# Kernel tuning notes

Hardware: AMD Instinct MI355X
Metric: run time of the kernel (lower is better)

Reference implementation:

```python
import jax, jax.numpy as jnp
import numpy as np

N = 50000
E = 800000
H = 8
DH = 32  # hidden 256 / heads 8


def gat_layer(h, src, dst, W, a_src, a_dst, b):
    # h: [N, 256] -> per-head projected features [N, H, DH]
    hp = (h @ W).reshape(N, H, DH)
    # per-node attention logits for src/dst roles: [N, H]
    s_src = jnp.einsum('nhd,hd->nh', hp, a_src)
    s_dst = jnp.einsum('nhd,hd->nh', hp, a_dst)
    e = jax.nn.leaky_relu(s_src[src] + s_dst[dst], negative_slope=0.2)  # [Et, H]
    # segment softmax over incoming edges of each dst node
    m = jax.ops.segment_max(e, dst, num_segments=N)  # [N, H]
    ex = jnp.exp(e - m[dst])
    denom = jax.ops.segment_sum(ex, dst, num_segments=N)  # [N, H] (>0: self-loops)
    alpha = ex / denom[dst]  # [Et, H]
    out = jax.ops.segment_sum(alpha[:, :, None] * hp[src], dst, num_segments=N)
    return out.reshape(N, H * DH) + b


def han_forward(x, edges, proj_W, proj_b, gat_W, gat_asrc, gat_adst, gat_b,
                sem_W1, sem_b1, sem_W2, cls_W1, cls_b1, cls_W2, cls_b2):
    h0 = x @ proj_W + proj_b  # [N, 256]
    loop = jnp.arange(N, dtype=edges.dtype)
    embs = []
    for p in range(edges.shape[0]):  # 3 meta-paths (fixed, small)
        src = jnp.concatenate([edges[p, 0], loop])  # add self-loops (PyG default)
        dst = jnp.concatenate([edges[p, 1], loop])
        h = h0
        for l in range(2):  # 2 GAT layers per meta-path
            h = gat_layer(h, src, dst, gat_W[p, l], gat_asrc[p, l], gat_adst[p, l], gat_b[p, l])
            h = jax.nn.elu(h)  # dropout: eval-mode no-op
        embs.append(h)
    emb = jnp.stack(embs, axis=1)  # [N, P, 256]
    scores = (jnp.tanh(emb @ sem_W1 + sem_b1) @ sem_W2).squeeze(-1)  # [N, P]
    w = jax.nn.softmax(scores, axis=1)
    z = jnp.sum(emb * w[:, :, None], axis=1)  # [N, 256]
    hcls = jax.nn.relu(z @ cls_W1 + cls_b1)
    logits = hcls @ cls_W2 + cls_b2  # [N, 2]
    return logits


def setup_inputs() -> dict:
    key = jax.random.key(0)
    ks = jax.random.split(key, 16)
    s = 0.05
    return {
        'x': jax.random.normal(ks[0], (N, 128), jnp.float32),
        'edges': jax.random.randint(ks[1], (3, 2, E), 0, N, dtype=jnp.int32),
        'proj_W': jax.random.normal(ks[2], (128, 256), jnp.float32) * s,
        'proj_b': jnp.zeros((256,), jnp.float32),
        'gat_W': jax.random.normal(ks[3], (3, 2, 256, 256), jnp.float32) * s,
        'gat_asrc': jax.random.normal(ks[4], (3, 2, H, DH), jnp.float32) * s,
        'gat_adst': jax.random.normal(ks[5], (3, 2, H, DH), jnp.float32) * s,
        'gat_b': jnp.zeros((3, 2, 256), jnp.float32),
        'sem_W1': jax.random.normal(ks[6], (256, 128), jnp.float32) * s,
        'sem_b1': jnp.zeros((128,), jnp.float32),
        'sem_W2': jax.random.normal(ks[7], (128, 1), jnp.float32) * s,
        'cls_W1': jax.random.normal(ks[8], (256, 128), jnp.float32) * s,
        'cls_b1': jnp.zeros((128,), jnp.float32),
        'cls_W2': jax.random.normal(ks[9], (128, 2), jnp.float32) * s,
        'cls_b2': jnp.zeros((2,), jnp.float32),
    }


def reference(x, edges, proj_W, proj_b, gat_W, gat_asrc, gat_adst, gat_b,
              sem_W1, sem_b1, sem_W2, cls_W1, cls_b1, cls_W2, cls_b2):
    return han_forward(x, edges, proj_W, proj_b, gat_W, gat_asrc, gat_adst, gat_b,
                       sem_W1, sem_b1, sem_W2, cls_W1, cls_b1, cls_W2, cls_b2)
```

## Files before the change

### kernel.cpp

```cpp
#include <hip/hip_runtime.h>
#include <hip/hip_fp16.h>
#include <math.h>

#define N_NODES 50000
#define N_EDG   800000
#define NH      8
#define DH      32
#define HID     256
#define MAXD    64
#define EPB     4096
#define PROJ_FB 88
#define PROJ_EB (176*EPB)
#define G3_FB   69
#define AGGB    12500

typedef __attribute__((ext_vector_type(8))) short bf16x8;
typedef __attribute__((ext_vector_type(4))) float f32x4;

#define GLL16(src, dst) __builtin_amdgcn_global_load_lds(                  \
    (const __attribute__((address_space(1))) void*)(const void*)(src),     \
    (__attribute__((address_space(3))) void*)(dst), 16, 0, 0)

__device__ __forceinline__ unsigned short f2bf(float x) {
    unsigned u = __float_as_uint(x);
    u += 0x7FFF + ((u >> 16) & 1);
    return (unsigned short)(u >> 16);
}
__device__ __forceinline__ float bf2f(unsigned short h) {
    return __uint_as_float(((unsigned)h) << 16);
}
__device__ __forceinline__ unsigned cvtpk_bf16(float a, float b) {
    unsigned r;
    asm("v_cvt_pk_bf16_f32 %0, %1, %2" : "=v"(r) : "v"(a), "v"(b));
    return r;
}
__device__ __forceinline__ float fastrcp(float x) {
    float r;
    asm("v_rcp_f32 %0, %1" : "=v"(r) : "v"(x));
    return r;
}
__device__ __forceinline__ void split8(const float4& a, const float4& b,
                                       uint4& hi, uint4& lo) {
    float f[8] = {a.x,a.y,a.z,a.w,b.x,b.y,b.z,b.w};
    unsigned hpk[4], lpk[4];
    #pragma unroll
    for (int i = 0; i < 4; ++i) {
        hpk[i] = cvtpk_bf16(f[2*i], f[2*i+1]);
        float hl = __uint_as_float(hpk[i] << 16);
        float hh = __uint_as_float(hpk[i] & 0xffff0000u);
        lpk[i] = cvtpk_bf16(f[2*i] - hl, f[2*i+1] - hh);
    }
    hi = make_uint4(hpk[0], hpk[1], hpk[2], hpk[3]);
    lo = make_uint4(lpk[0], lpk[1], lpk[2], lpk[3]);
}
__device__ __forceinline__ void h8_to_pair(uint4 r, uint4& hi, uint4& lo) {
    const __half2* hp = (const __half2*)&r;
    unsigned hpk[4], lpk[4];
    #pragma unroll
    for (int i = 0; i < 4; ++i) {
        float2 f = __half22float2(hp[i]);
        hpk[i] = cvtpk_bf16(f.x, f.y);
        float hl = __uint_as_float(hpk[i] << 16);
        float hh = __uint_as_float(hpk[i] & 0xffff0000u);
        lpk[i] = cvtpk_bf16(f.x - hl, f.y - hh);
    }
    hi = make_uint4(hpk[0], hpk[1], hpk[2], hpk[3]);
    lo = make_uint4(lpk[0], lpk[1], lpk[2], lpk[3]);
}

__device__ __forceinline__ void fmix2(float& alo, float& ahi, unsigned rv, float w) {
    asm("v_fma_mix_f32 %0, %1, %2, %0 op_sel:[0,0,0] op_sel_hi:[1,0,0]"
        : "+v"(alo) : "v"(rv), "v"(w));
    asm("v_fma_mix_f32 %0, %1, %2, %0 op_sel:[1,0,0] op_sel_hi:[1,0,0]"
        : "+v"(ahi) : "v"(rv), "v"(w));
}

__device__ __forceinline__ void fill_edges(const int* __restrict__ edges,
                                           int* __restrict__ cnt3,
                                           unsigned short* __restrict__ slots3,
                                           int fb, int ebase) {
    const int base = ebase + fb * EPB + (int)threadIdx.x;
    #pragma unroll 1
    for (int t = 0; t < 4; ++t) {
        int dd[4], ss[4];
        #pragma unroll
        for (int j = 0; j < 4; ++j) {
            int e = base + (t * 4 + j) * 256;
            if (e < 3 * N_EDG) {
                int p = e / N_EDG, i = e - p * N_EDG;
                const int* src = edges + (size_t)p * 2 * N_EDG;
                int s = src[i], d = src[N_EDG + i];
                ss[j] = min(max(s, 0), N_NODES - 1);
                dd[j] = p * N_NODES + min(max(d, 0), N_NODES - 1);
            } else { ss[j] = -1; dd[j] = 0; }
        }
        int pos[4];
        #pragma unroll
        for (int j = 0; j < 4; ++j)
            if (ss[j] >= 0) pos[j] = atomicAdd(&cnt3[dd[j]], 1);
        #pragma unroll
        for (int j = 0; j < 4; ++j)
            if (ss[j] >= 0 && pos[j] < MAXD)
                slots3[(size_t)dd[j] * MAXD + pos[j]] = (unsigned short)ss[j];
    }
}

__device__ __forceinline__ void agg_worker(
    int fb, int p, int l,
    const int* __restrict__ cnt3, const unsigned short* __restrict__ slots3,
    const float* __restrict__ ssrc3, const float* __restrict__ sdst3,
    const __half* __restrict__ hp3, const float* __restrict__ gatB,
    __half* __restrict__ emb16) {
    const int wid  = fb * 4 + ((int)threadIdx.x >> 6);
    const int lane = threadIdx.x & 63;
    if (wid >= N_NODES) return;
    const int n = wid;
    const unsigned short* srcs = slots3 + ((size_t)p * N_NODES + n) * MAXD;
    const float* s_src = ssrc3 + p * N_NODES * NH;
    const float* s_dst = sdst3 + p * N_NODES * NH;
    const __half* hp = hp3 + (size_t)p * N_NODES * HID;
    const float* bias = gatB + (2*p + l) * HID;
    const int deg = min(cnt3[p * N_NODES + n], MAXD);

    const int sub = lane & 31, eo = lane >> 5;
    const int h2  = sub >> 2;
    const float sd2 = s_dst[n*NH + h2];
    const uint4* hp4 = (const uint4*)hp;
    float dn = 0.f;
    float a0=0.f,a1=0.f,a2=0.f,a3=0.f,a4=0.f,a5=0.f,a6=0.f,a7=0.f;

    int i = eo;
    for (; i + 6 < deg; i += 8) {
        const int s0 = srcs[i];
        const int s1 = srcs[i + 2];
        const int s2 = srcs[i + 4];
        const int s3 = srcs[i + 6];
        const float x0 = s_src[s0*NH + h2];
        const float x1 = s_src[s1*NH + h2];
        const float x2 = s_src[s2*NH + h2];
        const float x3 = s_src[s3*NH + h2];
        const uint4 r0 = hp4[s0*32 + sub];
        const uint4 r1 = hp4[s1*32 + sub];
        const uint4 r2 = hp4[s2*32 + sub];
        const uint4 r3 = hp4[s3*32 + sub];
        float e0 = x0 + sd2; e0 = e0 > 0.f ? e0 : 0.2f * e0;
        float e1 = x1 + sd2; e1 = e1 > 0.f ? e1 : 0.2f * e1;
        float e2 = x2 + sd2; e2 = e2 > 0.f ? e2 : 0.2f * e2;
        float e3 = x3 + sd2; e3 = e3 > 0.f ? e3 : 0.2f * e3;
        const float w0 = __expf(e0), w1 = __expf(e1);
        const float w2 = __expf(e2), w3 = __expf(e3);
        dn += w0; dn += w1; dn += w2; dn += w3;
        fmix2(a0, a1, r0.x, w0); fmix2(a2, a3, r0.y, w0);
        fmix2(a4, a5, r0.z, w0); fmix2(a6, a7, r0.w, w0);
        fmix2(a0, a1, r1.x, w1); fmix2(a2, a3, r1.y, w1);
        fmix2(a4, a5, r1.z, w1); fmix2(a6, a7, r1.w, w1);
        fmix2(a0, a1, r2.x, w2); fmix2(a2, a3, r2.y, w2);
        fmix2(a4, a5, r2.z, w2); fmix2(a6, a7, r2.w, w2);
        fmix2(a0, a1, r3.x, w3); fmix2(a2, a3, r3.y, w3);
        fmix2(a4, a5, r3.z, w3); fmix2(a6, a7, r3.w, w3);
    }
    for (; i + 2 < deg; i += 4) {
        const int s0 = srcs[i];
        const int s1 = srcs[i + 2];
        const float x0 = s_src[s0*NH + h2];
        const float x1 = s_src[s1*NH + h2];
        const uint4 r0 = hp4[s0*32 + sub];
        const uint4 r1 = hp4[s1*32 + sub];
        float e0 = x0 + sd2; e0 = e0 > 0.f ? e0 : 0.2f * e0;
        float e1 = x1 + sd2; e1 = e1 > 0.f ? e1 : 0.2f * e1;
        const float w0 = __expf(e0), w1 = __expf(e1);
        dn += w0; dn += w1;
        fmix2(a0, a1, r0.x, w0); fmix2(a2, a3, r0.y, w0);
        fmix2(a4, a5, r0.z, w0); fmix2(a6, a7, r0.w, w0);
        fmix2(a0, a1, r1.x, w1); fmix2(a2, a3, r1.y, w1);
        fmix2(a4, a5, r1.z, w1); fmix2(a6, a7, r1.w, w1);
    }
    if (i < deg) {
        const int s0 = srcs[i];
        const float x0 = s_src[s0*NH + h2];
        const uint4 r0 = hp4[s0*32 + sub];
        float e0 = x0 + sd2; e0 = e0 > 0.f ? e0 : 0.2f * e0;
        const float w0 = __expf(e0);
        dn += w0;
        fmix2(a0, a1, r0.x, w0); fmix2(a2, a3, r0.y, w0);
        fmix2(a4, a5, r0.z, w0); fmix2(a6, a7, r0.w, w0);
    }
    dn += __shfl_xor(dn, 32);
    a0 += __shfl_xor(a0, 32); a1 += __shfl_xor(a1, 32);
    a2 += __shfl_xor(a2, 32); a3 += __shfl_xor(a3, 32);
    a4 += __shfl_xor(a4, 32); a5 += __shfl_xor(a5, 32);
    a6 += __shfl_xor(a6, 32); a7 += __shfl_xor(a7, 32);
    if (lane < 32) {
        float evs = s_src[n*NH + h2] + sd2;
        evs = evs > 0.f ? evs : 0.2f * evs;
        float ws = __expf(evs);
        dn += ws;
        const uint4 rs = hp4[n*32 + sub];
        fmix2(a0, a1, rs.x, ws); fmix2(a2, a3, rs.y, ws);
        fmix2(a4, a5, rs.z, ws); fmix2(a6, a7, rs.w, ws);

        float rdn = fastrcp(dn);
        float v[8] = {a0,a1,a2,a3,a4,a5,a6,a7};
        const float4 b0 = *(const float4*)&bias[sub*8];
        const float4 b1 = *(const float4*)&bias[sub*8 + 4];
        v[0]=v[0]*rdn+b0.x; v[1]=v[1]*rdn+b0.y; v[2]=v[2]*rdn+b0.z; v[3]=v[3]*rdn+b0.w;
        v[4]=v[4]*rdn+b1.x; v[5]=v[5]*rdn+b1.y; v[6]=v[6]*rdn+b1.z; v[7]=v[7]*rdn+b1.w;
        unsigned short hh[8];
        #pragma unroll
        for (int k = 0; k < 8; ++k) {
            float e = v[k] > 0.f ? v[k] : (__expf(v[k]) - 1.f);
            hh[k] = __half_as_ushort(__float2half(e));
        }
        size_t o = ((size_t)p * N_NODES + n) * HID + sub * 8;
        *(uint4*)&emb16[o] = make_uint4(hh[0]|((unsigned)hh[1]<<16), hh[2]|((unsigned)hh[3]<<16),
                                        hh[4]|((unsigned)hh[5]<<16), hh[6]|((unsigned)hh[7]<<16));
    }
}

__global__ __launch_bounds__(256)
void agg3y_k(const int* __restrict__ cnt3, const unsigned short* __restrict__ slots3,
             const float* __restrict__ ssrc3, const float* __restrict__ sdst3,
             const __half* __restrict__ hp3, const float* __restrict__ gatB,
             int l, __half* __restrict__ emb16) {
    agg_worker(blockIdx.x, blockIdx.y, l, cnt3, slots3, ssrc3, sdst3, hp3, gatB, emb16);
}

template<int NC, int ACT, int OUTMODE, int AMODE, int FILL>
__global__ __launch_bounds__(256)
void mfma_gemm_k(const float* __restrict__ A32p, const __half* __restrict__ A16p,
                 int lda,
                 const unsigned short* __restrict__ WThi,
                 const unsigned short* __restrict__ WTlo,
                 const float* __restrict__ bias,
                 float* __restrict__ C, __half* __restrict__ Ch,
                 int ldc, int M, int K,
                 const int* __restrict__ edges, int* __restrict__ cnt3,
                 unsigned short* __restrict__ slots3,
                 const float* __restrict__ w4z,
                 int aplanez, int cplanez,
                 const float* __restrict__ logW2, const float* __restrict__ logB2) {
    __shared__ unsigned short sAh[128*32], sAl[128*32], sBh[128*32], sBl[128*32];
    const int gxk = (M + 127) >> 7;
    if constexpr (FILL) {
        if ((int)blockIdx.x >= gxk) {
            fill_edges(edges, cnt3, slots3,
                       ((int)blockIdx.x - gxk) + PROJ_FB * (int)blockIdx.y, 0);
            return;
        }
    }
    if (A16p) A16p += (size_t)blockIdx.z * aplanez;
    if (C)    C    += (size_t)blockIdx.z * cplanez;
    const int tid  = threadIdx.x;
    const int lane = tid & 63;
    const int w    = tid >> 6;
    const int wr   = w >> 1, wc = w & 1;
    const int r0   = blockIdx.x * 128;
    const int c0   = blockIdx.y * 128;
    const int l15  = lane & 15, q = lane >> 4;

    const int cl8   = (((lane & 3) ^ ((lane >> 4) & 3)) << 3);
    const int lrow  = w*32 + (lane >> 2);
    const int gbrow0 = c0 + lrow, gbrow1 = c0 + lrow + 16;
    const int lbase = w * 1024;

    const int srow = tid >> 2, slot = tid & 3;
    const int arow0 = min(r0 + srow,      M - 1);
    const int arow1 = min(r0 + srow + 64, M - 1);
    const size_t ga0 = (size_t)arow0 * lda + slot * 8;
    const size_t ga1 = (size_t)arow1 * lda + slot * 8;
    const int lda0 = srow*32 + ((slot ^ ((srow >> 2) & 3)) << 3);
    const int lda1 = lda0 + 64*32;

    float4 w0r, w1r;
    if constexpr (AMODE == 3) {
        w0r = *(const float4*)&w4z[arow0 * 4];
        w1r = *(const float4*)&w4z[arow1 * 4];
    }

    f32x4 acc[4][4];
    #pragma unroll
    for (int i = 0; i < 4; ++i)
        #pragma unroll
        for (int j = 0; j < 4; ++j) acc[i][j] = (f32x4){0.f, 0.f, 0.f, 0.f};

    const int swzF = (l15 >> 2) & 3;
    const int qs   = ((q ^ swzF) << 3);

    const int nsteps = K >> 5;
    for (int s = 0; s < nsteps; ++s) {
        const int kc = s << 5;
        __syncthreads();
        GLL16(&WThi[(size_t)gbrow0*K + kc + cl8], &sBh[lbase]);
        GLL16(&WThi[(size_t)gbrow1*K + kc + cl8], &sBh[lbase + 512]);
        GLL16(&WTlo[(size_t)gbrow0*K + kc + cl8], &sBl[lbase]);
        GLL16(&WTlo[(size_t)gbrow1*K + kc + cl8], &sBl[lbase + 512]);
        uint4 h0, l0, h1, l1;
        if constexpr (AMODE == 0) {
            float4 f0a = *(const float4*)&A32p[ga0 + kc];
            float4 f0b = *(const float4*)&A32p[ga0 + kc + 4];
            float4 f1a = *(const float4*)&A32p[ga1 + kc];
            float4 f1b = *(const float4*)&A32p[ga1 + kc + 4];
            split8(f0a, f0b, h0, l0);
            split8(f1a, f1b, h1, l1);
        } else if constexpr (AMODE == 1) {
            uint4 r0v = *(const uint4*)&A16p[ga0 + kc];
            uint4 r1v = *(const uint4*)&A16p[ga1 + kc];
            h8_to_pair(r0v, h0, l0);
            h8_to_pair(r1v, h1, l1);
        } else {
            const int off = kc + slot * 8;
            #pragma unroll
            for (int rr = 0; rr < 2; ++rr) {
                const int row = rr ? arow1 : arow0;
                const float4 wv = rr ? w1r : w0r;
                const __half2* e0 = (const __half2*)&A16p[(size_t)row * HID + off];
                const __half2* e1 = (const __half2*)&A16p[((size_t)N_NODES + row) * HID + off];
                const __half2* e2 = (const __half2*)&A16p[((size_t)2*N_NODES + row) * HID + off];
                float vv[8];
                #pragma unroll
                for (int j2 = 0; j2 < 4; ++j2) {
                    float2 fa = __half22float2(e0[j2]);
                    float2 fb2 = __half22float2(e1[j2]);
                    float2 fc = __half22float2(e2[j2]);
                    vv[2*j2]   = wv.x*fa.x + wv.y*fb2.x + wv.z*fc.x;
                    vv[2*j2+1] = wv.x*fa.y + wv.y*fb2.y + wv.z*fc.y;
                }
                if (rr) split8(*(const float4*)&vv[0], *(const float4*)&vv[4], h1, l1);
                else    split8(*(const float4*)&vv[0], *(const float4*)&vv[4], h0, l0);
            }
        }
        *(uint4*)&sAh[lda0] = h0; *(uint4*)&sAl[lda0] = l0;
        *(uint4*)&sAh[lda1] = h1; *(uint4*)&sAl[lda1] = l1;
        __syncthreads();

        bf16x8 fAh[4], fAl[4];
        #pragma unroll
        for (int t = 0; t < 4; ++t) {
            int ra = (wr*64 + t*16 + l15) * 32 + qs;
            fAh[t] = *(const bf16x8*)&sAh[ra];
            fAl[t] = *(const bf16x8*)&sAl[ra];
        }
        #pragma unroll
        for (int nt = 0; nt < 4; ++nt) {
            int rb = (wc*64 + nt*16 + l15) * 32 + qs;
            bf16x8 fBh = *(const bf16x8*)&sBh[rb];
            bf16x8 fBl = *(const bf16x8*)&sBl[rb];
            #pragma unroll
            for (int mt = 0; mt < 4; ++mt) {
                acc[mt][nt] = __builtin_amdgcn_mfma_f32_16x16x32_bf16(fAh[mt], fBh, acc[mt][nt], 0, 0, 0);
                acc[mt][nt] = __builtin_amdgcn_mfma_f32_16x16x32_bf16(fAh[mt], fBl, acc[mt][nt], 0, 0, 0);
                acc[mt][nt] = __builtin_amdgcn_mfma_f32_16x16x32_bf16(fAl[mt], fBh, acc[mt][nt], 0, 0, 0);
            }
        }
    }
    if constexpr (OUTMODE == 3) {
        __syncthreads();
        float* red = (float*)sAh;
        float pl[16][2];
        #pragma unroll
        for (int mt = 0; mt < 4; ++mt)
            #pragma unroll
            for (int r = 0; r < 4; ++r) {
                float p0 = 0.f, p1 = 0.f;
                #pragma unroll
                for (int nt = 0; nt < 4; ++nt) {
                    int col = wc*64 + nt*16 + l15;
                    float v = fmaxf(acc[mt][nt][r] + bias[col], 0.f);
                    p0 += v * logW2[col*2];
                    p1 += v * logW2[col*2 + 1];
                }
                #pragma unroll
                for (int o = 1; o < 16; o <<= 1) {
                    p0 += __shfl_xor(p0, o);
                    p1 += __shfl_xor(p1, o);
                }
                pl[mt*4 + r][0] = p0;
                pl[mt*4 + r][1] = p1;
            }
        if (wc == 1 && l15 == 0) {
            #pragma unroll
            for (int mt = 0; mt < 4; ++mt)
                #pragma unroll
                for (int r = 0; r < 4; ++r) {
                    int rl = wr*64 + mt*16 + q*4 + r;
                    red[rl*2]     = pl[mt*4 + r][0];
                    red[rl*2 + 1] = pl[mt*4 + r][1];
                }
        }
        __syncthreads();
        if (wc == 0 && l15 == 0) {
            #pragma unroll
            for (int mt = 0; mt < 4; ++mt)
                #pragma unroll
                for (int r = 0; r < 4; ++r) {
                    int rl = wr*64 + mt*16 + q*4 + r;
                    int grow = r0 + rl;
                    if (grow < M) {
                        C[(size_t)grow*2]     = pl[mt*4+r][0] + red[rl*2]     + logB2[0];
                        C[(size_t)grow*2 + 1] = pl[mt*4+r][1] + red[rl*2 + 1] + logB2[1];
                    }
                }
        }
        return;
    }
    #pragma unroll
    for (int mt = 0; mt < 4; ++mt)
        #pragma unroll
        for (int nt = 0; nt < 4; ++nt) {
            int col = c0 + wc*64 + nt*16 + l15;
            float bb = bias ? bias[col] : 0.f;
            #pragma unroll
            for (int r = 0; r < 4; ++r) {
                int grow = r0 + wr*64 + mt*16 + q*4 + r;
                if (grow < M) {
                    float v = acc[mt][nt][r] + bb;
                    if (ACT == 1) {
                        float t = __expf(2.f * v);
                        v = 1.f - 2.f * fastrcp(1.f + t);
                    } else if (ACT == 2) v = fmaxf(v, 0.f);
                    size_t o = (size_t)grow * ldc + col;
                    if (OUTMODE == 2) Ch[o] = __float2half(v);
                    else              C[o] = v;
                }
            }
        }
}

template<int FILL>
__global__ __launch_bounds__(256)
void mfma_gemm3_k(const __half* __restrict__ A16p, int aoffz, int lda,
                  const unsigned short* __restrict__ WT, int l,
                  __half* __restrict__ hp3, int M,
                  const int* __restrict__ edges, int* __restrict__ cnt3,
                  unsigned short* __restrict__ slots3) {
    __shared__ unsigned short sAh[128*32], sAl[128*32], sBh[128*32], sBl[128*32];
    const int gx = (M + 127) >> 7;
    if constexpr (FILL) {
        if ((int)blockIdx.x >= gx) {
            fill_edges(edges, cnt3, slots3,
                       ((int)blockIdx.x - gx) + G3_FB * ((int)blockIdx.y + 2 * (int)blockIdx.z),
                       PROJ_EB);
            return;
        }
    }
    const int p = blockIdx.z;
    const __half* Ap = A16p + (size_t)p * aoffz;
    const unsigned short* WThi = WT + (size_t)(2*p + l) * 131072;
    const unsigned short* WTlo = WThi + 65536;
    __half* Ch = hp3 + (size_t)p * N_NODES * HID;
    const int K = HID;

    const int tid  = threadIdx.x;
    const int lane = tid & 63;
    const int w    = tid >> 6;
    const int wr   = w >> 1, wc = w & 1;
    const int r0   = blockIdx.x * 128;
    const int c0   = blockIdx.y * 128;
    const int l15  = lane & 15, q = lane >> 4;

    const int cl8   = (((lane & 3) ^ ((lane >> 4) & 3)) << 3);
    const int lrow  = w*32 + (lane >> 2);
    const int gbrow0 = c0 + lrow, gbrow1 = c0 + lrow + 16;
    const int lbase = w * 1024;

    const int srow = tid >> 2, slot = tid & 3;
    const size_t ga0 = (size_t)min(r0 + srow,      M - 1) * lda + slot * 8;
    const size_t ga1 = (size_t)min(r0 + srow + 64, M - 1) * lda + slot * 8;
    const int lda0 = srow*32 + ((slot ^ ((srow >> 2) & 3)) << 3);
    const int lda1 = lda0 + 64*32;

    f32x4 acc[4][4];
    #pragma unroll
    for (int i = 0; i < 4; ++i)
        #pragma unroll
        for (int j = 0; j < 4; ++j) acc[i][j] = (f32x4){0.f, 0.f, 0.f, 0.f};

    const int swzF = (l15 >> 2) & 3;
    const int qs   = ((q ^ swzF) << 3);

    for (int s = 0; s < 8; ++s) {
        const int kc = s << 5;
        __syncthreads();
        GLL16(&WThi[(size_t)gbrow0*K + kc + cl8], &sBh[lbase]);
        GLL16(&WThi[(size_t)gbrow1*K + kc + cl8], &sBh[lbase + 512]);
        GLL16(&WTlo[(size_t)gbrow0*K + kc + cl8], &sBl[lbase]);
        GLL16(&WTlo[(size_t)gbrow1*K + kc + cl8], &sBl[lbase + 512]);
        uint4 r0v = *(const uint4*)&Ap[ga0 + kc];
        uint4 r1v = *(const uint4*)&Ap[ga1 + kc];
        uint4 h0, l0, h1, l1;
        h8_to_pair(r0v, h0, l0);
        h8_to_pair(r1v, h1, l1);
        *(uint4*)&sAh[lda0] = h0; *(uint4*)&sAl[lda0] = l0;
        *(uint4*)&sAh[lda1] = h1; *(uint4*)&sAl[lda1] = l1;
        __syncthreads();

        bf16x8 fAh[4], fAl[4];
        #pragma unroll
        for (int t = 0; t < 4; ++t) {
            int ra = (wr*64 + t*16 + l15) * 32 + qs;
            fAh[t] = *(const bf16x8*)&sAh[ra];
            fAl[t] = *(const bf16x8*)&sAl[ra];
        }
        #pragma unroll
        for (int nt = 0; nt < 4; ++nt) {
            int rb = (wc*64 + nt*16 + l15) * 32 + qs;
            bf16x8 fBh = *(const bf16x8*)&sBh[rb];
            bf16x8 fBl = *(const bf16x8*)&sBl[rb];
            #pragma unroll
            for (int mt = 0; mt < 4; ++mt) {
                acc[mt][nt] = __builtin_amdgcn_mfma_f32_16x16x32_bf16(fAh[mt], fBh, acc[mt][nt], 0, 0, 0);
                acc[mt][nt] = __builtin_amdgcn_mfma_f32_16x16x32_bf16(fAh[mt], fBl, acc[mt][nt], 0, 0, 0);
                acc[mt][nt] = __builtin_amdgcn_mfma_f32_16x16x32_bf16(fAl[mt], fBh, acc[mt][nt], 0, 0, 0);
            }
        }
    }
    #pragma unroll
    for (int mt = 0; mt < 4; ++mt)
        #pragma unroll
        for (int nt = 0; nt < 4; ++nt) {
            int col = c0 + wc*64 + nt*16 + l15;
            #pragma unroll
            for (int r = 0; r < 4; ++r) {
                int grow = r0 + wr*64 + mt*16 + q*4 + r;
                if (grow < M)
                    Ch[(size_t)grow * HID + col] = __float2half(acc[mt][nt][r]);
            }
        }
}

__global__ __launch_bounds__(256)
void cvtWall_k(const float* __restrict__ gatW, const float* __restrict__ projW,
               const float* __restrict__ semW1, const float* __restrict__ clsW1,
               unsigned short* __restrict__ WT) {
    int y = blockIdx.y;
    const float* W; int K, N;
    if (y < 6)       { W = gatW + (size_t)y * 65536; K = 256; N = 256; }
    else if (y == 6) { W = projW; K = 128; N = 256; }
    else if (y == 7) { W = semW1; K = 256; N = 128; }
    else             { W = clsW1; K = 256; N = 128; }
    int idx = blockIdx.x * 256 + threadIdx.x;
    if (idx >= K * N) return;
    unsigned short* hi = WT + (size_t)y * 131072;
    unsigned short* lo = hi + 65536;
    int k = idx / N, n = idx - k * N;
    float v = W[idx];
    unsigned short h = f2bf(v);
    hi[n * K + k] = h;
    lo[n * K + k] = f2bf(v - bf2f(h));
}

__global__ __launch_bounds__(256)
void attn_scores3_k(const __half* __restrict__ hp3,
                    const float* __restrict__ gatAs, const float* __restrict__ gatAd,
                    int l, int pbase, float* __restrict__ ssrc3, float* __restrict__ sdst3) {
    int p = pbase + blockIdx.y;
    int gid = blockIdx.x * 256 + threadIdx.x;
    if (gid >= N_NODES * NH) return;
    int h = gid & 7;
    const __half2* hv = (const __half2*)(hp3 + (size_t)p * N_NODES * HID + (size_t)gid * DH);
    const float* a = gatAs + (2*p + l) * HID + h * DH;
    const float* d = gatAd + (2*p + l) * HID + h * DH;
    float ss = 0.f, sd = 0.f;
    #pragma unroll
    for (int j = 0; j < 8; ++j) {
        float4 av = ((const float4*)a)[j], dv = ((const float4*)d)[j];
        float2 f0 = __half22float2(hv[2*j]);
        float2 f1 = __half22float2(hv[2*j + 1]);
        ss += f0.x*av.x + f0.y*av.y + f1.x*av.z + f1.y*av.w;
        sd += f0.x*dv.x + f0.y*dv.y + f1.x*dv.z + f1.y*dv.w;
    }
    ssrc3[p * N_NODES * NH + gid] = ss;
    sdst3[p * N_NODES * NH + gid] = sd;
}

__global__ __launch_bounds__(256)
void zero_k(int* p, int n) { int i = blockIdx.x*256 + threadIdx.x; if (i < n) p[i] = 0; }

__global__ __launch_bounds__(256)
void score_w_k(const float* __restrict__ tb, const float* __restrict__ W2,
               float* __restrict__ w4) {
    int wid  = (blockIdx.x * blockDim.x + threadIdx.x) >> 6;
    int lane = threadIdx.x & 63;
    if (wid >= N_NODES) return;
    const int n = wid;
    float sc[3];
    #pragma unroll
    for (int p = 0; p < 3; ++p) {
        const float* tr = tb + (size_t)p * N_NODES * 128 + (size_t)n * 128;
        float part = tr[lane] * W2[lane] + tr[64 + lane] * W2[64 + lane];
        #pragma unroll
        for (int o = 1; o < 64; o <<= 1) part += __shfl_xor(part, o);
        sc[p] = part;
    }
    float m  = fmaxf(sc[0], fmaxf(sc[1], sc[2]));
    float e0 = __expf(sc[0]-m), e1 = __expf(sc[1]-m), e2 = __expf(sc[2]-m);
    float rs = fastrcp(e0 + e1 + e2);
    if (lane == 0)
        *(float4*)&w4[(size_t)n * 4] = make_float4(e0*rs, e1*rs, e2*rs, 0.f);
}

extern "C" void kernel_launch(void* const* d_in, const int* in_sizes, int n_in,
                              void* d_out, int out_size, void* d_ws, size_t ws_size,
                              hipStream_t stream) {
    (void)in_sizes; (void)n_in; (void)out_size; (void)ws_size;
    const float* x     = (const float*)d_in[0];
    const int*   edges = (const int*)  d_in[1];
    const float* projW = (const float*)d_in[2];
    const float* projb = (const float*)d_in[3];
    const float* gatW  = (const float*)d_in[4];
    const float* gatAs = (const float*)d_in[5];
    const float* gatAd = (const float*)d_in[6];
    const float* gatB  = (const float*)d_in[7];
    const float* semW1 = (const float*)d_in[8];
    const float* semb1 = (const float*)d_in[9];
    const float* semW2 = (const float*)d_in[10];
    const float* clsW1 = (const float*)d_in[11];
    const float* clsb1 = (const float*)d_in[12];
    const float* clsW2 = (const float*)d_in[13];
    const float* clsb2 = (const float*)d_in[14];
    float* out = (float*)d_out;

    char* base = (char*)d_ws;
    const size_t PLANE = (size_t)N_NODES * HID * 2;
    __half* hp3   = (__half*)(base);
    __half* emb16 = (__half*)(base + 3*PLANE);
    __half* h016  = (__half*)(base + 6*PLANE);
    char* small = base + 7*PLANE;
    float* ssrc3 = (float*)small;
    float* sdst3 = ssrc3 + 3*(size_t)N_NODES*NH;
    int*   cnt3  = (int*)(sdst3 + 3*(size_t)N_NODES*NH);
    unsigned short* WT = (unsigned short*)(cnt3 + 3*N_NODES);
    unsigned short* slots3 = WT + 9*131072;
    float* w4 = (float*)(slots3 + (size_t)3*N_NODES*MAXD);
    float* t0 = (float*)(base);

    dim3 blk(256);
    const int gx = (N_NODES + 127) / 128;

    cvtWall_k<<<dim3(256, 9), blk, 0, stream>>>(gatW, projW, semW1, clsW1, WT);
    zero_k  <<<(3*N_NODES+255)/256, blk, 0, stream>>>(cnt3, 3*N_NODES);

    mfma_gemm_k<256,0,2,0,1><<<dim3(gx + PROJ_FB, 2), blk, 0, stream>>>(
        x, nullptr, 128, WT + 6*131072, WT + 6*131072 + 65536, projb,
        nullptr, h016, 256, N_NODES, 128, edges, cnt3, slots3, nullptr, 0, 0,
        nullptr, nullptr);

    mfma_gemm3_k<1><<<dim3(gx + G3_FB, 2, 3), blk, 0, stream>>>(
        h016, 0, HID, WT, 0, hp3, N_NODES, edges, cnt3, slots3);

    attn_scores3_k<<<dim3((N_NODES*NH+255)/256, 3), blk, 0, stream>>>(
        hp3, gatAs, gatAd, 0, 0, ssrc3, sdst3);

    agg3y_k<<<dim3(AGGB, 3), blk, 0, stream>>>(
        cnt3, slots3, ssrc3, sdst3, hp3, gatB, 0, emb16);

    mfma_gemm3_k<0><<<dim3(gx, 2, 3), blk, 0, stream>>>(
        emb16, (int)((size_t)N_NODES*HID), HID, WT, 1, hp3, N_NODES,
        nullptr, nullptr, nullptr);

    attn_scores3_k<<<dim3((N_NODES*NH+255)/256, 3), blk, 0, stream>>>(
        hp3, gatAs, gatAd, 1, 0, ssrc3, sdst3);

    agg3y_k<<<dim3(AGGB, 3), blk, 0, stream>>>(
        cnt3, slots3, ssrc3, sdst3, hp3, gatB, 1, emb16);

    mfma_gemm_k<128,1,0,1,0><<<dim3(gx, 1, 3), blk, 0, stream>>>(
        nullptr, emb16, 256, WT + 7*131072, WT + 7*131072 + 65536, semb1,
        t0, nullptr, 128, N_NODES, 256, nullptr, nullptr, nullptr, nullptr,
        (int)((size_t)N_NODES*HID), N_NODES*128, nullptr, nullptr);

    score_w_k<<<dim3(AGGB), blk, 0, stream>>>(t0, semW2, w4);

    mfma_gemm_k<128,2,3,3,0><<<dim3(gx, 1), blk, 0, stream>>>(
        nullptr, emb16, HID, WT + 8*131072, WT + 8*131072 + 65536, clsb1,
        out, nullptr, 0, N_NODES, 256, nullptr, nullptr, nullptr, w4, 0, 0,
        clsW2, clsb2);
}
```

Measured before the change: 942.3 us.

## Fuse attention-score dots into GAT GEMM epilogue and semantic score into sem GEMM

Per-head attention logits (s_src, s_dst) are now computed from the fp32 accumulators in the GAT projection GEMM epilogue with shuffle reductions, which removes the separate attn_scores kernel that re-read the fp16 hp3 planes. The semantic-attention GEMM gains an epilogue that applies tanh, dots with sem_W2 and reduces across the two column waves through LDS. It writes one score per node and metapath straight into w4, replacing the [N,128] intermediate and the wave-per-node score kernel with a small softmax kernel. Scores are now taken from unrounded fp32 accumulators rather than fp16 values, which changes numerics slightly, and the extra epilogue work adds register pressure to the GEMMs.

```diff
diff --git a/kernel.cpp b/kernel.cpp
--- a/kernel.cpp
+++ b/kernel.cpp
@@ -403,6 +403,48 @@
         }
         return;
     }
+    if constexpr (OUTMODE == 4) {
+        __syncthreads();
+        float* red = (float*)sAh;
+        float pl[16];
+        #pragma unroll
+        for (int mt = 0; mt < 4; ++mt)
+            #pragma unroll
+            for (int r = 0; r < 4; ++r) {
+                float pp = 0.f;
+                #pragma unroll
+                for (int nt = 0; nt < 4; ++nt) {
+                    int col = wc*64 + nt*16 + l15;
+                    float v = acc[mt][nt][r] + bias[col];
+                    float t = __expf(2.f * v);
+                    v = 1.f - 2.f * fastrcp(1.f + t);
+                    pp += v * logW2[col];
+                }
+                #pragma unroll
+                for (int o = 1; o < 16; o <<= 1) pp += __shfl_xor(pp, o);
+                pl[mt*4 + r] = pp;
+            }
+        if (wc == 1 && l15 == 0) {
+            #pragma unroll
+            for (int mt = 0; mt < 4; ++mt)
+                #pragma unroll
+                for (int r = 0; r < 4; ++r)
+                    red[wr*64 + mt*16 + q*4 + r] = pl[mt*4 + r];
+        }
+        __syncthreads();
+        if (wc == 0 && l15 == 0) {
+            #pragma unroll
+            for (int mt = 0; mt < 4; ++mt)
+                #pragma unroll
+                for (int r = 0; r < 4; ++r) {
+                    int rl = wr*64 + mt*16 + q*4 + r;
+                    int grow = r0 + rl;
+                    if (grow < M)
+                        C[(size_t)grow*4] = pl[mt*4+r] + red[rl];
+                }
+        }
+        return;
+    }
     #pragma unroll
     for (int mt = 0; mt < 4; ++mt)
         #pragma unroll
@@ -432,7 +474,9 @@
                   const unsigned short* __restrict__ WT, int l,
                   __half* __restrict__ hp3, int M,
                   const int* __restrict__ edges, int* __restrict__ cnt3,
-                  unsigned short* __restrict__ slots3) {
+                  unsigned short* __restrict__ slots3,
+                  const float* __restrict__ gatAs, const float* __restrict__ gatAd,
+                  float* __restrict__ ssrc3, float* __restrict__ sdst3) {
     __shared__ unsigned short sAh[128*32], sAl[128*32], sBh[128*32], sBl[128*32];
     const int gx = (M + 127) >> 7;
     if constexpr (FILL) {
@@ -526,6 +570,42 @@
                     Ch[(size_t)grow * HID + col] = __float2half(acc[mt][nt][r]);
             }
         }
+    {
+        const float* av = gatAs + (2*p + l) * HID;
+        const float* dvv = gatAd + (2*p + l) * HID;
+        float as_[4], ad_[4];
+        #pragma unroll
+        for (int nt = 0; nt < 4; ++nt) {
+            int col = c0 + wc*64 + nt*16 + l15;
+            as_[nt] = av[col];
+            ad_[nt] = dvv[col];
+        }
+        const int hb = (c0 + wc*64) >> 5;
+        #pragma unroll
+        for (int mt = 0; mt < 4; ++mt)
+            #pragma unroll
+            for (int r = 0; r < 4; ++r) {
+                float s0 = acc[mt][0][r]*as_[0] + acc[mt][1][r]*as_[1];
+                float s1 = acc[mt][2][r]*as_[2] + acc[mt][3][r]*as_[3];
+                float d0 = acc[mt][0][r]*ad_[0] + acc[mt][1][r]*ad_[1];
+                float d1 = acc[mt][2][r]*ad_[2] + acc[mt][3][r]*ad_[3];
+                #pragma unroll
+                for (int o = 1; o < 16; o <<= 1) {
+                    s0 += __shfl_xor(s0, o); s1 += __shfl_xor(s1, o);
+                    d0 += __shfl_xor(d0, o); d1 += __shfl_xor(d1, o);
+                }
+                if (l15 == 0) {
+                    int grow = r0 + wr*64 + mt*16 + q*4 + r;
+                    if (grow < M) {
+                        size_t ob = (size_t)p * N_NODES * NH + (size_t)grow * NH;
+                        ssrc3[ob + hb]     = s0;
+                        ssrc3[ob + hb + 1] = s1;
+                        sdst3[ob + hb]     = d0;
+                        sdst3[ob + hb + 1] = d1;
+                    }
+                }
+            }
+    }
 }
 
 __global__ __launch_bounds__(256)
@@ -550,53 +630,17 @@
 }
 
 __global__ __launch_bounds__(256)
-void attn_scores3_k(const __half* __restrict__ hp3,
-                    const float* __restrict__ gatAs, const float* __restrict__ gatAd,
-                    int l, int pbase, float* __restrict__ ssrc3, float* __restrict__ sdst3) {
-    int p = pbase + blockIdx.y;
-    int gid = blockIdx.x * 256 + threadIdx.x;
-    if (gid >= N_NODES * NH) return;
-    int h = gid & 7;
-    const __half2* hv = (const __half2*)(hp3 + (size_t)p * N_NODES * HID + (size_t)gid * DH);
-    const float* a = gatAs + (2*p + l) * HID + h * DH;
-    const float* d = gatAd + (2*p + l) * HID + h * DH;
-    float ss = 0.f, sd = 0.f;
-    #pragma unroll
-    for (int j = 0; j < 8; ++j) {
-        float4 av = ((const float4*)a)[j], dv = ((const float4*)d)[j];
-        float2 f0 = __half22float2(hv[2*j]);
-        float2 f1 = __half22float2(hv[2*j + 1]);
-        ss += f0.x*av.x + f0.y*av.y + f1.x*av.z + f1.y*av.w;
-        sd += f0.x*dv.x + f0.y*dv.y + f1.x*dv.z + f1.y*dv.w;
-    }
-    ssrc3[p * N_NODES * NH + gid] = ss;
-    sdst3[p * N_NODES * NH + gid] = sd;
-}
+void zero_k(int* p, int n) { int i = blockIdx.x*256 + threadIdx.x; if (i < n) p[i] = 0; }
 
 __global__ __launch_bounds__(256)
-void zero_k(int* p, int n) { int i = blockIdx.x*256 + threadIdx.x; if (i < n) p[i] = 0; }
-
-__global__ __launch_bounds__(256)
-void score_w_k(const float* __restrict__ tb, const float* __restrict__ W2,
-               float* __restrict__ w4) {
-    int wid  = (blockIdx.x * blockDim.x + threadIdx.x) >> 6;
-    int lane = threadIdx.x & 63;
-    if (wid >= N_NODES) return;
-    const int n = wid;
-    float sc[3];
-    #pragma unroll
-    for (int p = 0; p < 3; ++p) {
-        const float* tr = tb + (size_t)p * N_NODES * 128 + (size_t)n * 128;
-        float part = tr[lane] * W2[lane] + tr[64 + lane] * W2[64 + lane];
-        #pragma unroll
-        for (int o = 1; o < 64; o <<= 1) part += __shfl_xor(part, o);
-        sc[p] = part;
-    }
-    float m  = fmaxf(sc[0], fmaxf(sc[1], sc[2]));
-    float e0 = __expf(sc[0]-m), e1 = __expf(sc[1]-m), e2 = __expf(sc[2]-m);
+void softmax3_k(float* __restrict__ sc) {
+    int n = blockIdx.x*256 + threadIdx.x;
+    if (n >= N_NODES) return;
+    float4 s = *(float4*)&sc[(size_t)n*4];
+    float m = fmaxf(s.x, fmaxf(s.y, s.z));
+    float e0 = __expf(s.x - m), e1 = __expf(s.y - m), e2 = __expf(s.z - m);
     float rs = fastrcp(e0 + e1 + e2);
-    if (lane == 0)
-        *(float4*)&w4[(size_t)n * 4] = make_float4(e0*rs, e1*rs, e2*rs, 0.f);
+    *(float4*)&sc[(size_t)n*4] = make_float4(e0*rs, e1*rs, e2*rs, 0.f);
 }
 
 extern "C" void kernel_launch(void* const* d_in, const int* in_sizes, int n_in,
@@ -632,7 +676,6 @@
     unsigned short* WT = (unsigned short*)(cnt3 + 3*N_NODES);
     unsigned short* slots3 = WT + 9*131072;
     float* w4 = (float*)(slots3 + (size_t)3*N_NODES*MAXD);
-    float* t0 = (float*)(base);
 
     dim3 blk(256);
     const int gx = (N_NODES + 127) / 128;
@@ -646,30 +689,25 @@
         nullptr, nullptr);
 
     mfma_gemm3_k<1><<<dim3(gx + G3_FB, 2, 3), blk, 0, stream>>>(
-        h016, 0, HID, WT, 0, hp3, N_NODES, edges, cnt3, slots3);
-
-    attn_scores3_k<<<dim3((N_NODES*NH+255)/256, 3), blk, 0, stream>>>(
-        hp3, gatAs, gatAd, 0, 0, ssrc3, sdst3);
+        h016, 0, HID, WT, 0, hp3, N_NODES, edges, cnt3, slots3,
+        gatAs, gatAd, ssrc3, sdst3);
 
     agg3y_k<<<dim3(AGGB, 3), blk, 0, stream>>>(
         cnt3, slots3, ssrc3, sdst3, hp3, gatB, 0, emb16);
 
     mfma_gemm3_k<0><<<dim3(gx, 2, 3), blk, 0, stream>>>(
         emb16, (int)((size_t)N_NODES*HID), HID, WT, 1, hp3, N_NODES,
-        nullptr, nullptr, nullptr);
-
-    attn_scores3_k<<<dim3((N_NODES*NH+255)/256, 3), blk, 0, stream>>>(
-        hp3, gatAs, gatAd, 1, 0, ssrc3, sdst3);
+        nullptr, nullptr, nullptr, gatAs, gatAd, ssrc3, sdst3);
 
     agg3y_k<<<dim3(AGGB, 3), blk, 0, stream>>>(
         cnt3, slots3, ssrc3, sdst3, hp3, gatB, 1, emb16);
 
-    mfma_gemm_k<128,1,0,1,0><<<dim3(gx, 1, 3), blk, 0, stream>>>(
+    mfma_gemm_k<128,1,4,1,0><<<dim3(gx, 1, 3), blk, 0, stream>>>(
         nullptr, emb16, 256, WT + 7*131072, WT + 7*131072 + 65536, semb1,
-        t0, nullptr, 128, N_NODES, 256, nullptr, nullptr, nullptr, nullptr,
-        (int)((size_t)N_NODES*HID), N_NODES*128, nullptr, nullptr);
-
-    score_w_k<<<dim3(AGGB), blk, 0, stream>>>(t0, semW2, w4);
+        w4, nullptr, 0, N_NODES, 256, nullptr, nullptr, nullptr, nullptr,
+        (int)((size_t)N_NODES*HID), 1, semW2, nullptr);
+
+    softmax3_k<<<(N_NODES+255)/256, blk, 0, stream>>>(w4);
 
     mfma_gemm_k<128,2,3,3,0><<<dim3(gx, 1), blk, 0, stream>>>(
         nullptr, emb16, HID, WT + 8*131072, WT + 8*131072 + 65536, clsb1,
```

Result: faster. 879.5 us (-6.7%).
